# Optimization experiments

Hardware: AMD Instinct MI355X
Metric: run time of the kernel (lower is better)

The kernel has to match this reference:

```python
import jax, jax.numpy as jnp
import numpy as np

BATCH, SEQ, F_DIM, R_DIM, OUT_DIM = 128, 1024, 256, 64, 1024


def setup_inputs() -> dict:
    key = jax.random.key(0)
    k1, k2, k3, k4, k5 = jax.random.split(key, 5)
    fillers = jax.random.normal(k1, (BATCH, SEQ, F_DIM), dtype=jnp.float32)
    roles = jax.random.normal(k2, (BATCH, SEQ, R_DIM), dtype=jnp.float32)
    lengths = jax.random.randint(k3, (BATCH,), 0, SEQ, dtype=jnp.int64)
    # nn.Linear(filler_dim*role_dim, output_dim): weight (out, in), bias (out,)
    bound = 1.0 / np.sqrt(F_DIM * R_DIM)
    W = jax.random.uniform(k4, (OUT_DIM, F_DIM * R_DIM), minval=-bound, maxval=bound, dtype=jnp.float32)
    b = jax.random.uniform(k5, (OUT_DIM,), minval=-bound, maxval=bound, dtype=jnp.float32)
    return {"fillers": fillers, "roles": roles, "lengths": lengths, "W": W, "b": b}


def reference(fillers, roles, lengths, W, b):
    batch, seq_len, f_dim = fillers.shape
    r_dim = roles.shape[-1]
    # mask[b, s] = s < lengths[b]
    mask = (jnp.arange(seq_len)[None, :] < lengths[:, None]).astype(fillers.dtype)
    # Fuse mask into fillers, then contract over seq directly:
    # sum_s mask * (fillers[b,s,:] outer roles[b,s,:]) == (mask*fillers)^T @ roles per batch
    # Avoids materializing the (b, s, e, r) intermediate; same math as the torch module.
    tensor_sum = jnp.einsum('bse,bsr->ber', fillers * mask[:, :, None], roles)  # (b, e, r)
    tensor_flat = tensor_sum.reshape(batch, f_dim * r_dim)
    return tensor_flat @ W.T + b
```

## Files before the change

### kernel.cpp

```cpp
#include <hip/hip_runtime.h>
#include <hip/hip_bf16.h>

#define NB 128
#define NS 1024
#define NE 256
#define NR 64
#define NO 1024
#define NK (NE*NR)

typedef __attribute__((ext_vector_type(8))) short short8;
typedef __attribute__((ext_vector_type(4))) float float4v;
typedef __attribute__((ext_vector_type(4))) unsigned short ushort4v;
typedef __attribute__((ext_vector_type(8))) unsigned short ushort8v;

static __device__ inline unsigned short f2bf(float x) {
    union { float f; unsigned u; } v; v.f = x;
    unsigned r = v.u + 0x7fffu + ((v.u >> 16) & 1u);
    return (unsigned short)(r >> 16);
}
static __device__ inline float bf2f(unsigned short h) {
    union { unsigned u; float f; } v; v.u = ((unsigned)h) << 16;
    return v.f;
}
static __device__ inline unsigned pk(float lo, float hi) {
    union { __hip_bfloat162 h2; unsigned u; } v;
    v.h2.x = __float2bfloat16(lo);
    v.h2.y = __float2bfloat16(hi);
    return v.u;
}

#define NCH 4

__global__ __launch_bounds__(512, 4) void k1_mfma(
    const float* __restrict__ fillers, const float* __restrict__ roles,
    const int* __restrict__ lengths, unsigned short* __restrict__ parts)
{
    const int bid = blockIdx.x;
    const int b   = bid >> 2;
    const int ch  = bid & 3;
    const int len = lengths[b];
    const int tid = threadIdx.x;

    const int lane = tid & 63;
    const int wid  = tid >> 6;
    const int lrow = lane & 15;
    const int lgrp = lane >> 4;

    const int e0 = wid * 32;

    const int P      = (len + 1) >> 1;
    const int count  = (P > ch) ? ((P - ch + 3) >> 2) : 0;
    const int nsteps = (count + 15) >> 4;

    float4v acc[2][4];
    #pragma unroll
    for (int i = 0; i < 2; ++i)
        #pragma unroll
        for (int j = 0; j < 4; ++j)
            acc[i][j] = (float4v){0.f, 0.f, 0.f, 0.f};

    const float* fb = fillers + (size_t)b * NS * NE;
    const float* rb = roles   + (size_t)b * NS * NR;

    for (int t = 0; t < nsteps; ++t) {
        const int sbase = 128 * t + 32 * lgrp + 2 * ch;
        const int shi   = 128 * t + 121 + 2 * ch;

        float a0[8], a1[8], b0[8], b1[8], b2[8], b3[8];
        #pragma unroll
        for (int j = 0; j < 8; ++j) {
            const int s = sbase + ((j >> 1) << 3) + (j & 1);
            const float* fr = fb + (size_t)s * NE;
            const float* rr = rb + (size_t)s * NR;
            a0[j] = fr[e0 + lrow];
            a1[j] = fr[e0 + 16 + lrow];
            b0[j] = rr[lrow];
            b1[j] = rr[16 + lrow];
            b2[j] = rr[32 + lrow];
            b3[j] = rr[48 + lrow];
        }

        if (shi >= len) {
            #pragma unroll
            for (int j = 0; j < 8; ++j) {
                const int s = sbase + ((j >> 1) << 3) + (j & 1);
                const bool v = (s < len);
                a0[j] = v ? a0[j] : 0.f;  a1[j] = v ? a1[j] : 0.f;
                b0[j] = v ? b0[j] : 0.f;  b1[j] = v ? b1[j] : 0.f;
                b2[j] = v ? b2[j] : 0.f;  b3[j] = v ? b3[j] : 0.f;
            }
        }

        union { unsigned u[4]; short8 s8; } af[2], bf[4];
        #pragma unroll
        for (int jj = 0; jj < 4; ++jj) {
            af[0].u[jj] = pk(a0[2*jj], a0[2*jj+1]);
            af[1].u[jj] = pk(a1[2*jj], a1[2*jj+1]);
            bf[0].u[jj] = pk(b0[2*jj], b0[2*jj+1]);
            bf[1].u[jj] = pk(b1[2*jj], b1[2*jj+1]);
            bf[2].u[jj] = pk(b2[2*jj], b2[2*jj+1]);
            bf[3].u[jj] = pk(b3[2*jj], b3[2*jj+1]);
        }

        #pragma unroll
        for (int mf = 0; mf < 2; ++mf)
            #pragma unroll
            for (int nf = 0; nf < 4; ++nf)
                acc[mf][nf] = __builtin_amdgcn_mfma_f32_16x16x32_bf16(
                    af[mf].s8, bf[nf].s8, acc[mf][nf], 0, 0, 0);
    }

    unsigned short* pp = parts + (size_t)(ch * NB + b) * NK;
    #pragma unroll
    for (int mf = 0; mf < 2; ++mf) {
        #pragma unroll
        for (int nf = 0; nf < 4; ++nf) {
            const int r = nf * 16 + lrow;
            #pragma unroll
            for (int reg = 0; reg < 4; ++reg) {
                const int e = e0 + mf * 16 + lgrp * 4 + reg;
                pp[(size_t)e * NR + r] = f2bf(acc[mf][nf][reg]);
            }
        }
    }
}

__global__ __launch_bounds__(256) void k1b_reduce(
    const unsigned short* __restrict__ parts, unsigned short* __restrict__ tensor)
{
    const size_t i = ((size_t)blockIdx.x * 256 + threadIdx.x) * 8;
    float s[8] = {0.f,0.f,0.f,0.f,0.f,0.f,0.f,0.f};
    #pragma unroll
    for (int ch = 0; ch < NCH; ++ch) {
        ushort8v v = *(const ushort8v*)(parts + (size_t)ch * NB * NK + i);
        #pragma unroll
        for (int j = 0; j < 8; ++j)
            s[j] += bf2f(v[j]);
    }
    ushort8v o;
    #pragma unroll
    for (int j = 0; j < 8; ++j)
        o[j] = f2bf(s[j]);
    *(ushort8v*)(tensor + i) = o;
}

#define BN2 64
#define BK2 128
#define KSPLIT 32
#define KC2 (NK/KSPLIT)

__global__ __launch_bounds__(512) void k2_mfma(
    const unsigned short* __restrict__ A,
    const float* __restrict__ W,
    float* __restrict__ part)
{
    __shared__ unsigned short As[128 * BK2];
    __shared__ unsigned short Bs[BN2 * BK2];

    const int o0   = blockIdx.x * BN2;
    const int kz   = blockIdx.y;
    const int tid  = threadIdx.x;
    const int lane = tid & 63;
    const int wid  = tid >> 6;
    const int wm   = wid >> 1;
    const int wn   = wid & 1;
    const int lrow = lane & 15;
    const int lgrp = lane >> 4;

    float4v acc[2][2];
    #pragma unroll
    for (int i = 0; i < 2; ++i)
        #pragma unroll
        for (int j = 0; j < 2; ++j)
            acc[i][j] = (float4v){0.f, 0.f, 0.f, 0.f};

    for (int step = 0; step < KC2 / BK2; ++step) {
        const int kb = kz * KC2 + step * BK2;

        ushort8v av[4];
        #pragma unroll
        for (int i = 0; i < 4; ++i) {
            const int c = tid + 512 * i;
            const int r = c >> 4, c16 = c & 15;
            av[i] = *(const ushort8v*)(A + (size_t)r * NK + kb + c16 * 8);
        }
        float4 wv[4];
        #pragma unroll
        for (int i = 0; i < 4; ++i) {
            const int c = tid + 512 * i;
            const int r = c >> 5, c4 = c & 31;
            wv[i] = *(const float4*)(W + (size_t)(o0 + r) * NK + kb + c4 * 4);
        }

        __syncthreads();

        #pragma unroll
        for (int i = 0; i < 4; ++i) {
            const int c = tid + 512 * i;
            const int r = c >> 4, c16 = c & 15;
            const int byte = (r * 256 + c16 * 16) ^ ((r & 7) << 4);
            *(ushort8v*)((char*)As + byte) = av[i];
        }
        #pragma unroll
        for (int i = 0; i < 4; ++i) {
            const int c = tid + 512 * i;
            const int r = c >> 5, c4 = c & 31;
            ushort4v bv = { f2bf(wv[i].x), f2bf(wv[i].y), f2bf(wv[i].z), f2bf(wv[i].w) };
            const int byte = (r * 256 + c4 * 8) ^ ((r & 7) << 4);
            *(ushort4v*)((char*)Bs + byte) = bv;
        }

        __syncthreads();

        #pragma unroll
        for (int kk = 0; kk < BK2; kk += 32) {
            short8 af[2], bf[2];
            #pragma unroll
            for (int mf = 0; mf < 2; ++mf) {
                const int r = wm * 32 + mf * 16 + lrow;
                const int byte = (r * 256 + (kk + lgrp * 8) * 2) ^ ((r & 7) << 4);
                af[mf] = *(const short8*)((const char*)As + byte);
            }
            #pragma unroll
            for (int nf = 0; nf < 2; ++nf) {
                const int r = wn * 32 + nf * 16 + lrow;
                const int byte = (r * 256 + (kk + lgrp * 8) * 2) ^ ((r & 7) << 4);
                bf[nf] = *(const short8*)((const char*)Bs + byte);
            }
            #pragma unroll
            for (int mf = 0; mf < 2; ++mf)
                #pragma unroll
                for (int nf = 0; nf < 2; ++nf)
                    acc[mf][nf] = __builtin_amdgcn_mfma_f32_16x16x32_bf16(
                        af[mf], bf[nf], acc[mf][nf], 0, 0, 0);
        }
    }

    float* pbase = part + (size_t)kz * NB * NO;
    #pragma unroll
    for (int mf = 0; mf < 2; ++mf) {
        #pragma unroll
        for (int nf = 0; nf < 2; ++nf) {
            const int o = o0 + wn * 32 + nf * 16 + lrow;
            #pragma unroll
            for (int reg = 0; reg < 4; ++reg) {
                const int m = wm * 32 + mf * 16 + lgrp * 4 + reg;
                pbase[(size_t)m * NO + o] = acc[mf][nf][reg];
            }
        }
    }
}

__global__ __launch_bounds__(256) void k3_reduce(
    const float* __restrict__ part, const float* __restrict__ bias,
    float* __restrict__ out)
{
    const int i = (blockIdx.x * 256 + threadIdx.x) * 4;
    float4 v = *(const float4*)(bias + (i & (NO - 1)));
    #pragma unroll
    for (int z = 0; z < KSPLIT; ++z) {
        float4 p = *(const float4*)(part + (size_t)z * NB * NO + i);
        v.x += p.x; v.y += p.y; v.z += p.z; v.w += p.w;
    }
    *(float4*)(out + i) = v;
}

extern "C" void kernel_launch(void* const* d_in, const int* in_sizes, int n_in,
                              void* d_out, int out_size, void* d_ws, size_t ws_size,
                              hipStream_t stream)
{
    const float* fillers = (const float*)d_in[0];
    const float* roles   = (const float*)d_in[1];
    const int*   lengths = (const int*)d_in[2];
    const float* W       = (const float*)d_in[3];
    const float* bias    = (const float*)d_in[4];
    float* out = (float*)d_out;

    unsigned short* tensor = (unsigned short*)d_ws;
    unsigned short* parts  = tensor + (size_t)NB * NK;
    float*          part   = (float*)parts;

    k1_mfma<<<NB * NCH, 512, 0, stream>>>(fillers, roles, lengths, parts);
    k1b_reduce<<<(NB * NK / 8) / 256, 256, 0, stream>>>(parts, tensor);
    dim3 g2(NO / BN2, KSPLIT);
    k2_mfma<<<g2, 512, 0, stream>>>(tensor, W, part);
    k3_reduce<<<(NB * NO) / 1024, 256, 0, stream>>>(part, bias, out);
}
```

Measured before the change: 55.25 us.

## Split sequence into eight chunks per batch and stage loads in halves

After: 59.71 us. +8.1%, slower.

```diff
diff --git a/kernel.cpp b/kernel.cpp
--- a/kernel.cpp
+++ b/kernel.cpp
@@ -29,15 +29,15 @@
     return v.u;
 }
 
-#define NCH 4
-
-__global__ __launch_bounds__(512, 4) void k1_mfma(
+#define NCH 8
+
+__global__ __launch_bounds__(512) void k1_mfma(
     const float* __restrict__ fillers, const float* __restrict__ roles,
     const int* __restrict__ lengths, unsigned short* __restrict__ parts)
 {
     const int bid = blockIdx.x;
-    const int b   = bid >> 2;
-    const int ch  = bid & 3;
+    const int b   = bid >> 3;
+    const int ch  = bid & 7;
     const int len = lengths[b];
     const int tid = threadIdx.x;
 
@@ -49,7 +49,7 @@
     const int e0 = wid * 32;
 
     const int P      = (len + 1) >> 1;
-    const int count  = (P > ch) ? ((P - ch + 3) >> 2) : 0;
+    const int count  = (P > ch) ? ((P - ch + 7) >> 3) : 0;
     const int nsteps = (count + 15) >> 4;
 
     float4v acc[2][4];
@@ -63,43 +63,47 @@
     const float* rb = roles   + (size_t)b * NS * NR;
 
     for (int t = 0; t < nsteps; ++t) {
-        const int sbase = 128 * t + 32 * lgrp + 2 * ch;
-        const int shi   = 128 * t + 121 + 2 * ch;
-
-        float a0[8], a1[8], b0[8], b1[8], b2[8], b3[8];
-        #pragma unroll
-        for (int j = 0; j < 8; ++j) {
-            const int s = sbase + ((j >> 1) << 3) + (j & 1);
-            const float* fr = fb + (size_t)s * NE;
-            const float* rr = rb + (size_t)s * NR;
-            a0[j] = fr[e0 + lrow];
-            a1[j] = fr[e0 + 16 + lrow];
-            b0[j] = rr[lrow];
-            b1[j] = rr[16 + lrow];
-            b2[j] = rr[32 + lrow];
-            b3[j] = rr[48 + lrow];
-        }
-
-        if (shi >= len) {
-            #pragma unroll
-            for (int j = 0; j < 8; ++j) {
-                const int s = sbase + ((j >> 1) << 3) + (j & 1);
-                const bool v = (s < len);
-                a0[j] = v ? a0[j] : 0.f;  a1[j] = v ? a1[j] : 0.f;
-                b0[j] = v ? b0[j] : 0.f;  b1[j] = v ? b1[j] : 0.f;
-                b2[j] = v ? b2[j] : 0.f;  b3[j] = v ? b3[j] : 0.f;
-            }
-        }
+        const int sb0 = 256 * t + 64 * lgrp + 2 * ch;
 
         union { unsigned u[4]; short8 s8; } af[2], bf[4];
-        #pragma unroll
-        for (int jj = 0; jj < 4; ++jj) {
-            af[0].u[jj] = pk(a0[2*jj], a0[2*jj+1]);
-            af[1].u[jj] = pk(a1[2*jj], a1[2*jj+1]);
-            bf[0].u[jj] = pk(b0[2*jj], b0[2*jj+1]);
-            bf[1].u[jj] = pk(b1[2*jj], b1[2*jj+1]);
-            bf[2].u[jj] = pk(b2[2*jj], b2[2*jj+1]);
-            bf[3].u[jj] = pk(b3[2*jj], b3[2*jj+1]);
+
+        #pragma unroll
+        for (int h = 0; h < 2; ++h) {
+            float a0[4], a1[4], b0[4], b1[4], b2[4], b3[4];
+            #pragma unroll
+            for (int j = 0; j < 4; ++j) {
+                const int v = 2 * h + (j >> 1);
+                const int s = sb0 + 16 * v + (j & 1);
+                const float* fr = fb + (size_t)s * NE;
+                const float* rr = rb + (size_t)s * NR;
+                a0[j] = fr[e0 + lrow];
+                a1[j] = fr[e0 + 16 + lrow];
+                b0[j] = rr[lrow];
+                b1[j] = rr[16 + lrow];
+                b2[j] = rr[32 + lrow];
+                b3[j] = rr[48 + lrow];
+            }
+            const int shi = 256 * t + 2 * ch + 192 + 16 * (2 * h + 1) + 1;
+            if (shi >= len) {
+                #pragma unroll
+                for (int j = 0; j < 4; ++j) {
+                    const int s = sb0 + 16 * (2 * h + (j >> 1)) + (j & 1);
+                    const bool ok = (s < len);
+                    a0[j] = ok ? a0[j] : 0.f;  a1[j] = ok ? a1[j] : 0.f;
+                    b0[j] = ok ? b0[j] : 0.f;  b1[j] = ok ? b1[j] : 0.f;
+                    b2[j] = ok ? b2[j] : 0.f;  b3[j] = ok ? b3[j] : 0.f;
+                }
+            }
+            #pragma unroll
+            for (int v = 0; v < 2; ++v) {
+                const int w = 2 * h + v;
+                af[0].u[w] = pk(a0[2*v], a0[2*v+1]);
+                af[1].u[w] = pk(a1[2*v], a1[2*v+1]);
+                bf[0].u[w] = pk(b0[2*v], b0[2*v+1]);
+                bf[1].u[w] = pk(b1[2*v], b1[2*v+1]);
+                bf[2].u[w] = pk(b2[2*v], b2[2*v+1]);
+                bf[3].u[w] = pk(b3[2*v], b3[2*v+1]);
+            }
         }
 
         #pragma unroll
```
